# Kernel tuning notes

Measured on AMD Instinct MI355X. Metric: run time of the kernel, lower is better.

Reference implementation:

```python
import jax, jax.numpy as jnp
import numpy as np

D_MODEL = 2048
D_HIDDEN = 2048
NUM_EXPERTS = 16
TOP_K = 2
N_TOKENS = 8192


def setup_inputs() -> dict:
    key = jax.random.key(0)
    k1, k2, k3 = jax.random.split(key, 3)
    x = jax.random.normal(k1, (N_TOKENS, D_MODEL), dtype=jnp.float32)
    router_weight = jax.random.normal(k2, (NUM_EXPERTS, D_MODEL), dtype=jnp.float32) * 0.02
    expert_weight = jax.random.normal(k3, (NUM_EXPERTS, D_MODEL, D_HIDDEN), dtype=jnp.float32) * 0.02
    return {"x": x, "router_weight": router_weight, "expert_weight": expert_weight}


def reference(x, router_weight, expert_weight):
    # Router: logits [N, E], top-k per token, softmax over selected logits
    logits = x @ router_weight.T
    top_logits, indices = jax.lax.top_k(logits, TOP_K)
    gates = jax.nn.softmax(top_logits, axis=-1)  # [N, K]

    n, e = logits.shape
    d_hidden = expert_weight.shape[2]
    # Dense per-token gate matrix [N, E]: zero for unselected experts
    dense_gate = jnp.zeros((n, e), dtype=x.dtype).at[
        jnp.arange(n)[:, None], indices
    ].add(gates)

    # out[t] = sum_e g[t,e] * (x[t] @ W[e]); scan over the small expert dim
    def body(acc, we_ge):
        w_e, g_e = we_ge  # [D, H], [N]
        return acc + (x * g_e[:, None]) @ w_e, None

    init = jnp.zeros((n, d_hidden), dtype=x.dtype)
    out, _ = jax.lax.scan(body, init, (expert_weight, dense_gate.T))
    return out
```

## Files before the change

### kernel.cpp

```cpp
#include <hip/hip_runtime.h>

#define NT 8192
#define DM 2048
#define DH 2048
#define NE 16
#define CSTRIDE 16

typedef __attribute__((ext_vector_type(8))) short short8;
typedef __attribute__((ext_vector_type(4))) float floatx4;

__device__ __forceinline__ unsigned short f2bf(float f){
  union { float f; unsigned u; } c; c.f = f;
  unsigned r = 0x7FFFu + ((c.u >> 16) & 1u);
  return (unsigned short)((c.u + r) >> 16);
}
__device__ __forceinline__ unsigned pk(float lo, float hi){
  return ((unsigned)f2bf(hi) << 16) | (unsigned)f2bf(lo);
}

__device__ __forceinline__ void gload_lds16(const void* g, void* l){
  __builtin_amdgcn_global_load_lds(
      (__attribute__((address_space(1))) void*)(unsigned long long)g,
      (__attribute__((address_space(3))) void*)l, 16, 0, 0);
}

__global__ __launch_bounds__(256) void cvt_kernel(
    const float4* __restrict__ src, uint2* __restrict__ dst, int n4)
{
  int i = blockIdx.x * 256 + threadIdx.x;
  if (i < n4){
    float4 v = src[i];
    dst[i] = make_uint2(pk(v.x, v.y), pk(v.z, v.w));
  }
}

__global__ __launch_bounds__(256) void cvt_wt_kernel(
    const float* __restrict__ w, unsigned short* __restrict__ wt)
{
  __shared__ unsigned short t[64][72];
  const int e = blockIdx.z;
  const int h0 = blockIdx.x * 64, d0 = blockIdx.y * 64;
  const size_t ib = (size_t)e * DM * DH;
  const int r = threadIdx.x >> 2;
  const int c = (threadIdx.x & 3) * 16;
  const float4* src = (const float4*)(w + ib + (size_t)(d0 + r) * DH + h0 + c);
  #pragma unroll
  for (int i = 0; i < 4; i++){
    float4 v = src[i];
    t[c+i*4+0][r] = f2bf(v.x);
    t[c+i*4+1][r] = f2bf(v.y);
    t[c+i*4+2][r] = f2bf(v.z);
    t[c+i*4+3][r] = f2bf(v.w);
  }
  __syncthreads();
  uint4* dst = (uint4*)(wt + ib + (size_t)(h0 + r) * DM + d0 + c);
  dst[0] = *(const uint4*)&t[r][c];
  dst[1] = *(const uint4*)&t[r][c+8];
}

__global__ __launch_bounds__(256) void router_kernel(
    const float* __restrict__ x,
    const float* __restrict__ rw,
    int* __restrict__ cnt,
    int* __restrict__ tok,
    float* __restrict__ gate)
{
  const int tid = threadIdx.x;
  const int s = tid & 31;
  const int t = blockIdx.x * 8 + (tid >> 5);
  const float* xrow = x + (size_t)t * DM;

  float lg[NE];
  #pragma unroll
  for (int e = 0; e < NE; e++) lg[e] = 0.f;

  #pragma unroll
  for (int i = 0; i < DM/128; i++){
    const int k = i*128 + s*4;
    float4 xv = *(const float4*)&xrow[k];
    #pragma unroll
    for (int e = 0; e < NE; e++){
      float4 wv = *(const float4*)&rw[e*DM + k];
      lg[e] += xv.x*wv.x + xv.y*wv.y + xv.z*wv.z + xv.w*wv.w;
    }
  }

  #pragma unroll
  for (int e = 0; e < NE; e++){
    #pragma unroll
    for (int o = 16; o > 0; o >>= 1) lg[e] += __shfl_xor(lg[e], o, 64);
  }

  if (s == 0){
    int i1 = 0; float v1 = lg[0];
    #pragma unroll
    for (int e = 1; e < NE; e++) if (lg[e] > v1){ v1 = lg[e]; i1 = e; }
    int i2 = -1; float v2 = -3.4e38f;
    #pragma unroll
    for (int e = 0; e < NE; e++) if (e != i1 && lg[e] > v2){ v2 = lg[e]; i2 = e; }
    float ex = __expf(v2 - v1);
    float g1 = 1.f / (1.f + ex);
    float g2 = ex / (1.f + ex);
    int p1 = atomicAdd(&cnt[i1*CSTRIDE], 1);
    tok[i1*NT + p1] = t;  gate[i1*NT + p1] = g1;
    int p2 = atomicAdd(&cnt[i2*CSTRIDE], 1);
    tok[i2*NT + p2] = t;  gate[i2*NT + p2] = g2;
  }
}

template<bool BF16>
__global__ __launch_bounds__(256) void moe_gemm(
    const float* __restrict__ xf, const unsigned short* __restrict__ xb,
    const float* __restrict__ wf, const unsigned short* __restrict__ wt,
    const int* __restrict__ cnt,
    const int* __restrict__ tok,
    const float* __restrict__ gate,
    float* __restrict__ out)
{
  constexpr int BM = 128, BN = 128, BK = 64;
  const int e = blockIdx.z;
  const int count = cnt[e*CSTRIDE];
  const int m0 = blockIdx.y * BM;
  if (m0 >= count) return;
  const int n0 = blockIdx.x * BN;
  const int tid = threadIdx.x;
  const int wave = tid >> 6, lane = tid & 63;

  const int* tokE = tok + e*NT;
  const float* gateE = gate + e*NT;
  const int mB = (wave & 1) * 64, nB = (wave >> 1) * 64;
  const int lrow = lane & 15, lgrp = lane >> 4;

  floatx4 acc[4][4];
  #pragma unroll
  for (int i = 0; i < 4; i++)
    #pragma unroll
    for (int j = 0; j < 4; j++) acc[i][j] = (floatx4){0.f, 0.f, 0.f, 0.f};

  if constexpr (BF16){
    __shared__ __align__(16) unsigned short As[BM*BK];
    __shared__ __align__(16) unsigned short Bs[BN*BK];

    const int kcs = ((lane & 7) ^ (lane >> 3)) * 8;
    const unsigned short* sA[4];
    const unsigned short* sB[4];
    #pragma unroll
    for (int i = 0; i < 4; i++){
      const int row = (wave*4 + i)*8 + (lane >> 3);
      int gr = m0 + row; if (gr > count - 1) gr = count - 1;
      sA[i] = xb + (size_t)tokE[gr]*DM + kcs;
      sB[i] = wt + ((size_t)e*DH + n0 + row)*DM + kcs;
    }

    for (int s = 0; s < DM/BK; s++){
      const int k0 = s * BK;
      if (s) __syncthreads();
      #pragma unroll
      for (int i = 0; i < 4; i++) gload_lds16(sA[i] + k0, &As[(wave*4 + i)*512]);
      #pragma unroll
      for (int i = 0; i < 4; i++) gload_lds16(sB[i] + k0, &Bs[(wave*4 + i)*512]);
      __syncthreads();

      #pragma unroll
      for (int kk = 0; kk < 2; kk++){
        short8 af[4], bfr[4];
        #pragma unroll
        for (int i = 0; i < 4; i++){
          const int row = mB + i*16 + lrow;
          af[i]  = *(const short8*)&As[row*64 + (((kk*4 + lgrp) ^ (row & 7)) * 8)];
        }
        #pragma unroll
        for (int j = 0; j < 4; j++){
          const int row = nB + j*16 + lrow;
          bfr[j] = *(const short8*)&Bs[row*64 + (((kk*4 + lgrp) ^ (row & 7)) * 8)];
        }
        #pragma unroll
        for (int i = 0; i < 4; i++)
          #pragma unroll
          for (int j = 0; j < 4; j++)
            acc[i][j] = __builtin_amdgcn_mfma_f32_16x16x32_bf16(af[i], bfr[j], acc[i][j], 0, 0, 0);
      }
    }
  } else {
    constexpr int LDK = 72;
    __shared__ __align__(16) unsigned short As[BM][LDK];
    __shared__ __align__(16) unsigned short Bs[BN][LDK];

    const int srowA = tid >> 3;
    const int kcA   = tid & 7;
    const int hp = tid & 31;
    const int dp = tid >> 5;

    int tokr[4];
    #pragma unroll
    for (int it = 0; it < 4; it++){
      int gr = m0 + srowA + it*32;
      if (gr > count - 1) gr = count - 1;
      tokr[it] = tokE[gr];
    }
    const size_t ebase = (size_t)e * DM * DH;

    float4 raf[8];
    float4 rbf[8];
    unsigned rbw[16];

    #pragma unroll
    for (int it = 0; it < 4; it++){
      const float4* p = (const float4*)&xf[(size_t)tokr[it]*DM + kcA*8];
      raf[it*2] = p[0]; raf[it*2+1] = p[1];
    }
    #pragma unroll
    for (int r = 0; r < 8; r++)
      rbf[r] = *(const float4*)&wf[ebase + (size_t)(dp*8 + r)*DH + n0 + hp*4];

    constexpr int S = DM / BK;
    for (int s = 0; s < S; s++){
      __syncthreads();
      #pragma unroll
      for (int it = 0; it < 4; it++){
        uint4 u;
        u.x = pk(raf[it*2].x,   raf[it*2].y);
        u.y = pk(raf[it*2].z,   raf[it*2].w);
        u.z = pk(raf[it*2+1].x, raf[it*2+1].y);
        u.w = pk(raf[it*2+1].z, raf[it*2+1].w);
        *(uint4*)&As[srowA + it*32][kcA*8] = u;
      }
      #pragma unroll
      for (int r = 0; r < 8; r++){
        rbw[r*2]   = pk(rbf[r].x, rbf[r].y);
        rbw[r*2+1] = pk(rbf[r].z, rbf[r].w);
      }
      #pragma unroll
      for (int j = 0; j < 4; j++){
        const unsigned sel = (j & 1) ? 0x07060302u : 0x05040100u;
        const int half = j >> 1;
        uint4 wv;
        wv.x = __builtin_amdgcn_perm(rbw[1*2+half], rbw[0*2+half], sel);
        wv.y = __builtin_amdgcn_perm(rbw[3*2+half], rbw[2*2+half], sel);
        wv.z = __builtin_amdgcn_perm(rbw[5*2+half], rbw[4*2+half], sel);
        wv.w = __builtin_amdgcn_perm(rbw[7*2+half], rbw[6*2+half], sel);
        *(uint4*)&Bs[hp*4 + j][dp*8] = wv;
      }
      __syncthreads();
      if (s + 1 < S){
        const int k0 = (s + 1) * BK;
        #pragma unroll
        for (int it = 0; it < 4; it++){
          const float4* p = (const float4*)&xf[(size_t)tokr[it]*DM + k0 + kcA*8];
          raf[it*2] = p[0]; raf[it*2+1] = p[1];
        }
        #pragma unroll
        for (int r = 0; r < 8; r++)
          rbf[r] = *(const float4*)&wf[ebase + (size_t)(k0 + dp*8 + r)*DH + n0 + hp*4];
      }
      #pragma unroll
      for (int kk = 0; kk < 2; kk++){
        const int kof = kk*32 + lgrp*8;
        short8 af[4], bfr[4];
        #pragma unroll
        for (int i = 0; i < 4; i++) af[i]  = *(const short8*)&As[mB + i*16 + lrow][kof];
        #pragma unroll
        for (int j = 0; j < 4; j++) bfr[j] = *(const short8*)&Bs[nB + j*16 + lrow][kof];
        #pragma unroll
        for (int i = 0; i < 4; i++)
          #pragma unroll
          for (int j = 0; j < 4; j++)
            acc[i][j] = __builtin_amdgcn_mfma_f32_16x16x32_bf16(af[i], bfr[j], acc[i][j], 0, 0, 0);
      }
    }
  }

  #pragma unroll
  for (int i = 0; i < 4; i++){
    #pragma unroll
    for (int r = 0; r < 4; r++){
      const int rloc = mB + i*16 + lgrp*4 + r;
      const int gr = m0 + rloc;
      if (gr < count){
        const int t = tokE[gr];
        const float g = gateE[gr];
        float* orow = out + (size_t)t*DH + n0 + nB;
        #pragma unroll
        for (int j = 0; j < 4; j++)
          atomicAdd(&orow[j*16 + lrow], acc[i][j][r] * g);
      }
    }
  }
}

extern "C" void kernel_launch(void* const* d_in, const int* in_sizes, int n_in,
                              void* d_out, int out_size, void* d_ws, size_t ws_size,
                              hipStream_t stream) {
  const float* x  = (const float*)d_in[0];
  const float* rw = (const float*)d_in[1];
  const float* w  = (const float*)d_in[2];
  float* out = (float*)d_out;

  char* ws = (char*)d_ws;
  int* cnt = (int*)ws;
  int* tok = (int*)(ws + 1024);
  float* gate = (float*)(ws + 1024 + (size_t)NE*NT*4);
  const size_t base = 1024 + (size_t)2*NE*NT*4;
  unsigned short* xb = (unsigned short*)(ws + base);
  unsigned short* wt = (unsigned short*)(ws + base + (size_t)NT*DM*2);
  const bool fast = ws_size >= base + (size_t)NT*DM*2 + (size_t)NE*DM*DH*2;

  hipMemsetAsync(cnt, 0, NE*CSTRIDE*sizeof(int), stream);
  hipMemsetAsync(out, 0, (size_t)NT*DH*sizeof(float), stream);
  router_kernel<<<NT/8, 256, 0, stream>>>(x, rw, cnt, tok, gate);

  dim3 gg(DH/128, NT/128, NE);
  if (fast){
    cvt_kernel<<<(NT*DM/4 + 255)/256, 256, 0, stream>>>((const float4*)x, (uint2*)xb, NT*DM/4);
    cvt_wt_kernel<<<dim3(DH/64, DM/64, NE), 256, 0, stream>>>(w, wt);
    moe_gemm<true ><<<gg, 256, 0, stream>>>(x, xb, w, wt, cnt, tok, gate, out);
  } else {
    moe_gemm<false><<<gg, 256, 0, stream>>>(x, xb, w, wt, cnt, tok, gate, out);
  }
}
```

Baseline: 815.6 us.

## Split top-k routing into two passes with plain stores; fuse x conversion into router

Routing lists are split by top-1 and top-2 slot. Each token then appears exactly once per pass, so the first GEMM pass writes output directly and the second pass does a read-add-write instead of atomicAdd. This removes the output memset and the float atomics. The x-to-bf16 conversion moves into the router kernel, which already reads x. The weight transpose kernel gets a wider 128-wide tile with an XOR-swizzled LDS layout and 16-byte stores. The cost is two GEMM launches that run in sequence, plus an extra read of the output in the second pass.

New measurement: 810.6 us. About the same (-0.6%).

```diff
diff --git a/kernel.cpp b/kernel.cpp
--- a/kernel.cpp
+++ b/kernel.cpp
@@ -24,43 +24,47 @@
       (__attribute__((address_space(3))) void*)l, 16, 0, 0);
 }
 
-__global__ __launch_bounds__(256) void cvt_kernel(
-    const float4* __restrict__ src, uint2* __restrict__ dst, int n4)
-{
-  int i = blockIdx.x * 256 + threadIdx.x;
-  if (i < n4){
-    float4 v = src[i];
-    dst[i] = make_uint2(pk(v.x, v.y), pk(v.z, v.w));
-  }
-}
-
 __global__ __launch_bounds__(256) void cvt_wt_kernel(
     const float* __restrict__ w, unsigned short* __restrict__ wt)
 {
-  __shared__ unsigned short t[64][72];
+  __shared__ __align__(16) unsigned short t[64*128];
   const int e = blockIdx.z;
-  const int h0 = blockIdx.x * 64, d0 = blockIdx.y * 64;
+  const int h0 = blockIdx.x * 64, d0 = blockIdx.y * 128;
   const size_t ib = (size_t)e * DM * DH;
-  const int r = threadIdx.x >> 2;
-  const int c = (threadIdx.x & 3) * 16;
-  const float4* src = (const float4*)(w + ib + (size_t)(d0 + r) * DH + h0 + c);
-  #pragma unroll
-  for (int i = 0; i < 4; i++){
-    float4 v = src[i];
-    t[c+i*4+0][r] = f2bf(v.x);
-    t[c+i*4+1][r] = f2bf(v.y);
-    t[c+i*4+2][r] = f2bf(v.z);
-    t[c+i*4+3][r] = f2bf(v.w);
+  const int hq = threadIdx.x & 15;
+  const int dg = threadIdx.x >> 4;
+
+  float4 v[8];
+  #pragma unroll
+  for (int r = 0; r < 8; r++)
+    v[r] = *(const float4*)&w[ib + (size_t)(d0 + dg*8 + r)*DH + h0 + hq*4];
+
+  const float* f = (const float*)v;
+  #pragma unroll
+  for (int hh = 0; hh < 4; hh++){
+    uint4 u;
+    u.x = pk(f[0*4+hh], f[1*4+hh]);
+    u.y = pk(f[2*4+hh], f[3*4+hh]);
+    u.z = pk(f[4*4+hh], f[5*4+hh]);
+    u.w = pk(f[6*4+hh], f[7*4+hh]);
+    const int h = hq*4 + hh;
+    *(uint4*)&t[h*128 + ((dg ^ (h & 7)) * 8)] = u;
   }
   __syncthreads();
-  uint4* dst = (uint4*)(wt + ib + (size_t)(h0 + r) * DM + d0 + c);
-  dst[0] = *(const uint4*)&t[r][c];
-  dst[1] = *(const uint4*)&t[r][c+8];
-}
-
+  #pragma unroll
+  for (int j = 0; j < 4; j++){
+    const int idx = j*256 + threadIdx.x;
+    const int h = idx >> 4, c = idx & 15;
+    uint4 u = *(const uint4*)&t[h*128 + ((c ^ (h & 7)) * 8)];
+    *(uint4*)&wt[ib + (size_t)(h0 + h)*DM + d0 + c*8] = u;
+  }
+}
+
+template<bool WX>
 __global__ __launch_bounds__(256) void router_kernel(
     const float* __restrict__ x,
     const float* __restrict__ rw,
+    unsigned short* __restrict__ xb,
     int* __restrict__ cnt,
     int* __restrict__ tok,
     float* __restrict__ gate)
@@ -78,6 +82,8 @@
   for (int i = 0; i < DM/128; i++){
     const int k = i*128 + s*4;
     float4 xv = *(const float4*)&xrow[k];
+    if (WX)
+      *(uint2*)&xb[(size_t)t*DM + k] = make_uint2(pk(xv.x, xv.y), pk(xv.z, xv.w));
     #pragma unroll
     for (int e = 0; e < NE; e++){
       float4 wv = *(const float4*)&rw[e*DM + k];
@@ -103,12 +109,12 @@
     float g2 = ex / (1.f + ex);
     int p1 = atomicAdd(&cnt[i1*CSTRIDE], 1);
     tok[i1*NT + p1] = t;  gate[i1*NT + p1] = g1;
-    int p2 = atomicAdd(&cnt[i2*CSTRIDE], 1);
-    tok[i2*NT + p2] = t;  gate[i2*NT + p2] = g2;
-  }
-}
-
-template<bool BF16>
+    int p2 = atomicAdd(&cnt[(NE + i2)*CSTRIDE], 1);
+    tok[(NE + i2)*NT + p2] = t;  gate[(NE + i2)*NT + p2] = g2;
+  }
+}
+
+template<bool ADD, bool BF16>
 __global__ __launch_bounds__(256) void moe_gemm(
     const float* __restrict__ xf, const unsigned short* __restrict__ xb,
     const float* __restrict__ wf, const unsigned short* __restrict__ wt,
@@ -281,8 +287,12 @@
         const float g = gateE[gr];
         float* orow = out + (size_t)t*DH + n0 + nB;
         #pragma unroll
-        for (int j = 0; j < 4; j++)
-          atomicAdd(&orow[j*16 + lrow], acc[i][j][r] * g);
+        for (int j = 0; j < 4; j++){
+          float v = acc[i][j][r] * g;
+          const int col = j*16 + lrow;
+          if (ADD) v += orow[col];
+          orow[col] = v;
+        }
       }
     }
   }
@@ -298,23 +308,24 @@
 
   char* ws = (char*)d_ws;
   int* cnt = (int*)ws;
-  int* tok = (int*)(ws + 1024);
-  float* gate = (float*)(ws + 1024 + (size_t)NE*NT*4);
-  const size_t base = 1024 + (size_t)2*NE*NT*4;
+  int* tok = (int*)(ws + 2048);
+  float* gate = (float*)(ws + 2048 + (size_t)2*NE*NT*4);
+  const size_t base = 2048 + (size_t)4*NE*NT*4;
   unsigned short* xb = (unsigned short*)(ws + base);
   unsigned short* wt = (unsigned short*)(ws + base + (size_t)NT*DM*2);
   const bool fast = ws_size >= base + (size_t)NT*DM*2 + (size_t)NE*DM*DH*2;
 
-  hipMemsetAsync(cnt, 0, NE*CSTRIDE*sizeof(int), stream);
-  hipMemsetAsync(out, 0, (size_t)NT*DH*sizeof(float), stream);
-  router_kernel<<<NT/8, 256, 0, stream>>>(x, rw, cnt, tok, gate);
+  hipMemsetAsync(cnt, 0, 2*NE*CSTRIDE*sizeof(int), stream);
 
   dim3 gg(DH/128, NT/128, NE);
   if (fast){
-    cvt_kernel<<<(NT*DM/4 + 255)/256, 256, 0, stream>>>((const float4*)x, (uint2*)xb, NT*DM/4);
-    cvt_wt_kernel<<<dim3(DH/64, DM/64, NE), 256, 0, stream>>>(w, wt);
-    moe_gemm<true ><<<gg, 256, 0, stream>>>(x, xb, w, wt, cnt, tok, gate, out);
+    router_kernel<true ><<<NT/8, 256, 0, stream>>>(x, rw, xb, cnt, tok, gate);
+    cvt_wt_kernel<<<dim3(DH/64, DM/128, NE), 256, 0, stream>>>(w, wt);
+    moe_gemm<false,true ><<<gg, 256, 0, stream>>>(x, xb, w, wt, cnt,             tok,       gate,       out);
+    moe_gemm<true ,true ><<<gg, 256, 0, stream>>>(x, xb, w, wt, cnt+NE*CSTRIDE,  tok+NE*NT, gate+NE*NT, out);
   } else {
-    moe_gemm<false><<<gg, 256, 0, stream>>>(x, xb, w, wt, cnt, tok, gate, out);
-  }
-}
+    router_kernel<false><<<NT/8, 256, 0, stream>>>(x, rw, xb, cnt, tok, gate);
+    moe_gemm<false,false><<<gg, 256, 0, stream>>>(x, xb, w, wt, cnt,             tok,       gate,       out);
+    moe_gemm<true ,false><<<gg, 256, 0, stream>>>(x, xb, w, wt, cnt+NE*CSTRIDE,  tok+NE*NT, gate+NE*NT, out);
+  }
+}
```
